# Optimization experiments

Measured on AMD Instinct MI355X. Metric: run time of the kernel, lower is better.

Reference implementation:

```python
import jax, jax.numpy as jnp
import numpy as np

N = 16384      # batch size
F = 1024       # n_features
H = 256        # n_dim (latent)


def setup_inputs() -> dict:
    key = jax.random.key(0)
    ks = jax.random.split(key, 6)
    X = jax.random.normal(ks[0], (N, F), dtype=jnp.float32)
    We = jax.random.normal(ks[1], (F, H), dtype=jnp.float32) / np.sqrt(F).astype(np.float32)
    be = jnp.zeros((H,), dtype=jnp.float32)
    Wd = jax.random.normal(ks[2], (H, F), dtype=jnp.float32) / np.sqrt(H).astype(np.float32)
    bd = jnp.zeros((F,), dtype=jnp.float32)
    Wc = jax.random.normal(ks[3], (H, 1), dtype=jnp.float32) / np.sqrt(H).astype(np.float32)
    bc = jnp.zeros((1,), dtype=jnp.float32)
    s = jax.random.randint(ks[4], (N,), 0, 2, dtype=jnp.int32)  # protected attribute labels in {0,1}
    return {"X": X, "We": We, "be": be, "Wd": Wd, "bd": bd, "Wc": Wc, "bc": bc, "s": s, "p": 1}


def reference(X, We, be, Wd, bd, Wc, bc, s, p):
    # encoder / decoder (single Linear each, as in the default NRL construction)
    g = X @ We + be                      # [N, H]
    rec = g @ Wd + bd                    # [N, F]
    mse_mean = jnp.mean((rec - X) ** 2)  # MSELoss is built with reduction='sum' but forward uses torch.mean(pow(...)) directly

    # critic scores for ALL rows (critics share weights: [module]*n_protected)
    c = (g @ Wc + bc)[:, 0]              # [N]

    # masked pairwise L1: sum_{i in P, j notin P} |c_i - c_j|
    mp = (s == p)                        # rows where s == p
    mpf = mp.astype(c.dtype)
    mrf = (~mp).astype(c.dtype)
    Dmat = jnp.abs(c[:, None] - c[None, :])   # [N, N] pairwise L1 (cdist equivalent)
    total = mpf @ (Dmat @ mrf)                # mp^T D mr == cdist(c_p, c_rest, p=1).sum()

    w_dist_count = mp.sum()                   # == w_dist.shape[0] (number of protected rows)
    w_dist_mean = total / w_dist_count.astype(c.dtype)

    return (mse_mean, jnp.asarray(rec.shape[0]), w_dist_mean, w_dist_count)
```

## Files before the change

kernel.cpp:

```cpp
#include <hip/hip_runtime.h>
#include <hip/hip_bf16.h>
#include <cstdint>

#define NR 16384
#define NF 1024
#define NH 256

typedef __bf16 bf16x8 __attribute__((ext_vector_type(8)));
typedef float f32x4 __attribute__((ext_vector_type(4)));
typedef unsigned short us8 __attribute__((ext_vector_type(8)));

static __device__ __forceinline__ unsigned short f2bf(float f) {
    unsigned u = __float_as_uint(f);
    u += 0x7FFFu + ((u >> 16) & 1u);
    return (unsigned short)(u >> 16);
}


__global__ __launch_bounds__(256) void prep_kernel(
    const float* __restrict__ We, const float* __restrict__ Wd,
    unsigned short* __restrict__ Wepk, unsigned short* __restrict__ Wdpk,
    float* __restrict__ hdr) {
    const int b = blockIdx.x, t = threadIdx.x;
    if (b == 0 && t < 192) hdr[t] = 0.f;
    const int lane = t & 63, q = lane >> 4, li = lane & 15, idx = t >> 6;
    if (b < 16) {
        const int nb = b;
#pragma unroll
        for (int p = 0; p < 8; p++) {
            const int kc = idx + 4 * p;
            us8 v;
#pragma unroll
            for (int e = 0; e < 8; e++)
                v[e] = f2bf(We[(size_t)(kc * 32 + q * 8 + e) * NH + nb * 16 + li]);
            *(us8*)&Wepk[((size_t)(nb * 32 + kc)) * 512 + lane * 8] = v;
        }
    } else {
        const int nb4 = b - 16;
#pragma unroll
        for (int p = 0; p < 8; p++) {
            const int c = nb4 * 32 + idx + 4 * p;
            const int nb = c >> 3, kc = c & 7;
            us8 v;
#pragma unroll
            for (int e = 0; e < 8; e++)
                v[e] = f2bf(Wd[(size_t)(kc * 32 + q * 8 + e) * NF + nb * 16 + li]);
            *(us8*)&Wdpk[((size_t)(nb * 8 + kc)) * 512 + lane * 8] = v;
        }
    }
}

__global__ __launch_bounds__(256) void fused_kernel(
    const float* __restrict__ X,
    const unsigned short* __restrict__ Wepk, const unsigned short* __restrict__ Wdpk,
    const float* __restrict__ be, const float* __restrict__ bd,
    const float* __restrict__ Wc, const int* __restrict__ s, const int* __restrict__ pv,
    float* __restrict__ cP, float* __restrict__ cR, float* __restrict__ hdr) {
    __shared__ union {
        unsigned short xa[16 * 1024];
        struct {
            unsigned short gs[16 * 256];
            float credu[4][16];
            float msred[4];
        } p2;
    } u;
    const int t = threadIdx.x;
    const int b = blockIdx.x, m0 = b * 16;
    const int w = t >> 6, lane = t & 63, q = lane >> 4, li = lane & 15;
    const int wn = w * 64;

    {
        const int r = t >> 4, cg = t & 15;
        const float* xrow = X + (size_t)(m0 + r) * NF + cg * 64;
#pragma unroll
        for (int ci = 0; ci < 8; ++ci) {
            float4 lo = *(const float4*)(xrow + ci * 8);
            float4 hi = *(const float4*)(xrow + ci * 8 + 4);
            us8 v;
            v[0] = f2bf(lo.x); v[1] = f2bf(lo.y); v[2] = f2bf(lo.z); v[3] = f2bf(lo.w);
            v[4] = f2bf(hi.x); v[5] = f2bf(hi.y); v[6] = f2bf(hi.z); v[7] = f2bf(hi.w);
            const int chl = cg * 8 + ci;
            *(us8*)&u.xa[r * 1024 + ((chl ^ r) & 127) * 8] = v;
        }
    }
    __syncthreads();

    const unsigned short* Bp[4];
#pragma unroll
    for (int j = 0; j < 4; j++)
        Bp[j] = Wepk + ((size_t)(w * 4 + j) * 32) * 512 + lane * 8;

    us8 fb[2][4];
#pragma unroll
    for (int z = 0; z < 2; ++z)
#pragma unroll
        for (int j = 0; j < 4; j++) fb[z][j] = *(const us8*)(Bp[j] + z * 512);

    f32x4 acc[4] = {};
#pragma unroll
    for (int kc = 0; kc < 32; ++kc) {
        const int cb = kc & 1;
        const int chl = kc * 4 + q;
        const int ph0 = (chl ^ li) & 127;
        bf16x8 a0 = __builtin_bit_cast(bf16x8, *(const us8*)&u.xa[li * 1024 + ph0 * 8]);
#pragma unroll
        for (int j = 0; j < 4; j++) {
            bf16x8 bf = __builtin_bit_cast(bf16x8, fb[cb][j]);
            acc[j] = __builtin_amdgcn_mfma_f32_16x16x32_bf16(bf, a0, acc[j], 0, 0, 0);
        }
        if (kc + 2 < 32) {
#pragma unroll
            for (int j = 0; j < 4; j++) fb[cb][j] = *(const us8*)(Bp[j] + (kc + 2) * 512);
        }
    }
    __syncthreads();

    const unsigned short* Wp = Wdpk + lane * 8;
    us8 gb[2][4];
#pragma unroll
    for (int z = 0; z < 2; ++z)
#pragma unroll
        for (int j = 0; j < 4; j++)
            gb[z][j] = *(const us8*)(Wp + ((size_t)((w * 4 + j) * 8 + z)) * 512);

    {
        float csum = 0.f;
        const int ml = li;
#pragma unroll
        for (int j = 0; j < 4; j++) {
            const int colb = wn + j * 16 + q * 4;
            float4 be4 = *(const float4*)&be[colb];
            float4 wc4 = *(const float4*)&Wc[colb];
            float v0 = acc[j][0] + be4.x;
            float v1 = acc[j][1] + be4.y;
            float v2 = acc[j][2] + be4.z;
            float v3 = acc[j][3] + be4.w;
            csum += v0 * wc4.x + v1 * wc4.y + v2 * wc4.z + v3 * wc4.w;
            ushort4 st = { f2bf(v0), f2bf(v1), f2bf(v2), f2bf(v3) };
            const int phys = (colb >> 3) ^ ml;
            *(ushort4*)&u.p2.gs[ml * 256 + phys * 8 + (q & 1) * 4] = st;
        }
        csum += __shfl_down(csum, 32);
        csum += __shfl_down(csum, 16);
        if (lane < 16) u.p2.credu[w][lane] = csum;
    }
    __syncthreads();

    if (t < 16) {
        float cs = u.p2.credu[0][t] + u.p2.credu[1][t] +
                   u.p2.credu[2][t] + u.p2.credu[3][t];
        bool pr = (s[m0 + t] == pv[0]);
        unsigned long long mk = __ballot(pr);
        int np = __popcll(mk);
        int baseP = 0, baseR = 0;
        if (t == 0) {
            baseP = atomicAdd((int*)hdr + 129, np);
            baseR = atomicAdd((int*)hdr + 130, 16 - np);
        }
        baseP = __shfl(baseP, 0);
        baseR = __shfl(baseR, 0);
        int offP = __popcll(mk & ((1ull << t) - 1ull));
        int offR = t - offP;
        if (pr) cP[baseP + offP] = cs; else cR[baseR + offR] = cs;
    }

    float lsum = 0.f;
    f32x4 a2[4] = {};
#pragma unroll
    for (int it = 0; it < 32; ++it) {
        const int cb = it & 1, pass = it >> 3, kc = it & 7;
        const int ml = li;
        const int phys = (kc * 4 + q) ^ ml;
        bf16x8 af = __builtin_bit_cast(bf16x8, *(const us8*)&u.p2.gs[ml * 256 + phys * 8]);
#pragma unroll
        for (int j = 0; j < 4; j++) {
            bf16x8 bf = __builtin_bit_cast(bf16x8, gb[cb][j]);
            a2[j] = __builtin_amdgcn_mfma_f32_16x16x32_bf16(bf, af, a2[j], 0, 0, 0);
        }
        if (it + 2 < 32) {
            const int p2i = (it + 2) >> 3, k2 = (it + 2) & 7;
#pragma unroll
            for (int j = 0; j < 4; j++)
                gb[cb][j] = *(const us8*)(Wp + ((size_t)((p2i * 16 + w * 4 + j) * 8 + k2)) * 512);
        }
        if (kc == 7) {
            const size_t rowoff = (size_t)(m0 + li) * NF;
#pragma unroll
            for (int j = 0; j < 4; j++) {
                const int colb = pass * 256 + wn + j * 16 + q * 4;
                float4 bd4 = *(const float4*)&bd[colb];
                float4 xr  = *(const float4*)&X[rowoff + colb];
                float d0 = a2[j][0] + bd4.x - xr.x;
                float d1 = a2[j][1] + bd4.y - xr.y;
                float d2 = a2[j][2] + bd4.z - xr.z;
                float d3 = a2[j][3] + bd4.w - xr.w;
                lsum += d0 * d0 + d1 * d1 + d2 * d2 + d3 * d3;
                a2[j] = (f32x4){0.f, 0.f, 0.f, 0.f};
            }
        }
    }
#pragma unroll
    for (int o = 32; o; o >>= 1) lsum += __shfl_down(lsum, o);
    if (lane == 0) u.p2.msred[w] = lsum;
    __syncthreads();
    if (t == 0)
        atomicAdd(&hdr[b & 63], u.p2.msred[0] + u.p2.msred[1] +
                                u.p2.msred[2] + u.p2.msred[3]);
}

__global__ __launch_bounds__(256) void pair_fin_kernel(
    const float* __restrict__ cP, const float* __restrict__ cR,
    float* __restrict__ hdr, float* __restrict__ out) {
    __shared__ float sj[1024];
    __shared__ float red[256];
    __shared__ int win;
    const int nP = ((const int*)hdr)[129];
    const int nR = ((const int*)hdr)[130];
    const int jb = blockIdx.x * 1024;
    int jn = nR - jb; if (jn < 0) jn = 0; if (jn > 1024) jn = 1024;
    float sum = 0.f;
    if (jn > 0 && blockIdx.y * 512 < nP) {
        for (int j = threadIdx.x; j < 1024; j += 256)
            sj[j] = (jb + j < nR) ? cR[jb + j] : 0.f;
        __syncthreads();
        const int a0 = blockIdx.y * 512 + threadIdx.x, a1 = a0 + 256;
        const float ca0 = (a0 < nP) ? cP[a0] : 0.f;
        const float ca1 = (a1 < nP) ? cP[a1] : 0.f;
        float s0 = 0.f, s1 = 0.f;
#pragma unroll 8
        for (int j4 = 0; j4 < 256; j4++) {
            float4 v = *(const float4*)&sj[j4 * 4];
            s0 += fabsf(ca0 - v.x) + fabsf(ca0 - v.y) + fabsf(ca0 - v.z) + fabsf(ca0 - v.w);
            s1 += fabsf(ca1 - v.x) + fabsf(ca1 - v.y) + fabsf(ca1 - v.z) + fabsf(ca1 - v.w);
        }
        float pad = (float)(1024 - jn);
        s0 -= pad * fabsf(ca0);
        s1 -= pad * fabsf(ca1);
        if (a0 >= nP) s0 = 0.f;
        if (a1 >= nP) s1 = 0.f;
        sum = s0 + s1;
#pragma unroll
        for (int o = 32; o; o >>= 1) sum += __shfl_down(sum, o);
        if ((threadIdx.x & 63) == 0 && sum != 0.f)
            atomicAdd(&hdr[64 + ((blockIdx.y * 16 + blockIdx.x) & 63)], sum);
    }
    __threadfence();
    __syncthreads();
    if (threadIdx.x == 0)
        win = (atomicAdd((int*)(hdr + 128), 1) == 16 * 32 - 1) ? 1 : 0;
    __syncthreads();
    if (win) {
        float v = (threadIdx.x < 128) ? atomicAdd(&hdr[threadIdx.x], 0.f) : 0.f;
        red[threadIdx.x] = v;
        __syncthreads();
        if (threadIdx.x == 0) {
            float ms = 0.f, ps = 0.f;
            for (int i = 0; i < 64; i++) { ms += red[i]; ps += red[64 + i]; }
            int np = atomicAdd((int*)(hdr + 129), 0);
            out[0] = ms / (float)((size_t)NR * NF);
            out[1] = (float)NR;
            out[2] = ps / (float)np;
            out[3] = (float)np;
        }
    }
}

extern "C" void kernel_launch(void* const* d_in, const int* in_sizes, int n_in,
                              void* d_out, int out_size, void* d_ws, size_t ws_size,
                              hipStream_t stream) {
    const float* X  = (const float*)d_in[0];
    const float* We = (const float*)d_in[1];
    const float* be = (const float*)d_in[2];
    const float* Wd = (const float*)d_in[3];
    const float* bd = (const float*)d_in[4];
    const float* Wc = (const float*)d_in[5];
    const int*   s  = (const int*)d_in[7];
    const int*   pv = (const int*)d_in[8];

    char* ws = (char*)d_ws;
    float* hdr = (float*)ws;
    float* cP  = (float*)(ws + 1024);
    float* cR  = (float*)(ws + 1024 + 65536);
    unsigned short* Wepk = (unsigned short*)(ws + 1024 + 2 * 65536);
    unsigned short* Wdpk = Wepk + (size_t)NH * NF;

    prep_kernel<<<32, 256, 0, stream>>>(We, Wd, Wepk, Wdpk, hdr);
    fused_kernel<<<1024, 256, 0, stream>>>(X, Wepk, Wdpk, be, bd, Wc, s, pv, cP, cR, hdr);
    pair_fin_kernel<<<dim3(16, 32), 256, 0, stream>>>(cP, cR, hdr, (float*)d_out);
}
```

Before: 214.4 us.

## Coalesce weight packing and X loads, deepen weight prefetch to four stages

The weight-packing kernel now runs 256 blocks, each thread handling one column, so global reads of We and Wd are coalesced across threads instead of strided. The X tile load is reorganized so each wave reads whole contiguous rows. In the fused kernel, the register prefetch ring for the packed weights grows from two to four stages to hide more global load latency. The deeper prefetch raises register pressure, which may reduce occupancy.

Measured after the change: 208.8 us. 2.6% less time.

```diff
diff --git a/kernel.cpp b/kernel.cpp
--- a/kernel.cpp
+++ b/kernel.cpp
@@ -23,30 +23,23 @@
     float* __restrict__ hdr) {
     const int b = blockIdx.x, t = threadIdx.x;
     if (b == 0 && t < 192) hdr[t] = 0.f;
-    const int lane = t & 63, q = lane >> 4, li = lane & 15, idx = t >> 6;
-    if (b < 16) {
-        const int nb = b;
-#pragma unroll
-        for (int p = 0; p < 8; p++) {
-            const int kc = idx + 4 * p;
-            us8 v;
-#pragma unroll
-            for (int e = 0; e < 8; e++)
-                v[e] = f2bf(We[(size_t)(kc * 32 + q * 8 + e) * NH + nb * 16 + li]);
-            *(us8*)&Wepk[((size_t)(nb * 32 + kc)) * 512 + lane * 8] = v;
-        }
+    if (b < 128) {
+        const int k0 = b, c = t;
+        const int kc = k0 >> 2, q = k0 & 3, nb = c >> 4, li = c & 15;
+        us8 v;
+#pragma unroll
+        for (int e = 0; e < 8; e++)
+            v[e] = f2bf(We[(size_t)(k0 * 8 + e) * NH + c]);
+        *(us8*)&Wepk[((size_t)(nb * 32 + kc)) * 512 + (q * 16 + li) * 8] = v;
     } else {
-        const int nb4 = b - 16;
-#pragma unroll
-        for (int p = 0; p < 8; p++) {
-            const int c = nb4 * 32 + idx + 4 * p;
-            const int nb = c >> 3, kc = c & 7;
-            us8 v;
-#pragma unroll
-            for (int e = 0; e < 8; e++)
-                v[e] = f2bf(Wd[(size_t)(kc * 32 + q * 8 + e) * NF + nb * 16 + li]);
-            *(us8*)&Wdpk[((size_t)(nb * 8 + kc)) * 512 + lane * 8] = v;
-        }
+        const int idx = b - 128;
+        const int k0 = idx >> 2, c = (idx & 3) * 256 + t;
+        const int kc = k0 >> 2, q = k0 & 3, nb = c >> 4, li = c & 15;
+        us8 v;
+#pragma unroll
+        for (int e = 0; e < 8; e++)
+            v[e] = f2bf(Wd[(size_t)(k0 * 8 + e) * NF + c]);
+        *(us8*)&Wdpk[((size_t)(nb * 8 + kc)) * 512 + (q * 16 + li) * 8] = v;
     }
 }
 
@@ -70,17 +63,20 @@
     const int wn = w * 64;
 
     {
-        const int r = t >> 4, cg = t & 15;
-        const float* xrow = X + (size_t)(m0 + r) * NF + cg * 64;
-#pragma unroll
-        for (int ci = 0; ci < 8; ++ci) {
-            float4 lo = *(const float4*)(xrow + ci * 8);
-            float4 hi = *(const float4*)(xrow + ci * 8 + 4);
-            us8 v;
-            v[0] = f2bf(lo.x); v[1] = f2bf(lo.y); v[2] = f2bf(lo.z); v[3] = f2bf(lo.w);
-            v[4] = f2bf(hi.x); v[5] = f2bf(hi.y); v[6] = f2bf(hi.z); v[7] = f2bf(hi.w);
-            const int chl = cg * 8 + ci;
-            *(us8*)&u.xa[r * 1024 + ((chl ^ r) & 127) * 8] = v;
+#pragma unroll
+        for (int rr = 0; rr < 4; ++rr) {
+            const int r = w * 4 + rr;
+            const float* xrow = X + (size_t)(m0 + r) * NF;
+#pragma unroll
+            for (int p = 0; p < 2; ++p) {
+                float4 lo = *(const float4*)(xrow + p * 512 + lane * 8);
+                float4 hi = *(const float4*)(xrow + p * 512 + lane * 8 + 4);
+                us8 v;
+                v[0] = f2bf(lo.x); v[1] = f2bf(lo.y); v[2] = f2bf(lo.z); v[3] = f2bf(lo.w);
+                v[4] = f2bf(hi.x); v[5] = f2bf(hi.y); v[6] = f2bf(hi.z); v[7] = f2bf(hi.w);
+                const int ch = p * 64 + lane;
+                *(us8*)&u.xa[r * 1024 + ((ch ^ r) & 127) * 8] = v;
+            }
         }
     }
     __syncthreads();
@@ -90,16 +86,16 @@
     for (int j = 0; j < 4; j++)
         Bp[j] = Wepk + ((size_t)(w * 4 + j) * 32) * 512 + lane * 8;
 
-    us8 fb[2][4];
-#pragma unroll
-    for (int z = 0; z < 2; ++z)
+    us8 fb[4][4];
+#pragma unroll
+    for (int z = 0; z < 4; ++z)
 #pragma unroll
         for (int j = 0; j < 4; j++) fb[z][j] = *(const us8*)(Bp[j] + z * 512);
 
     f32x4 acc[4] = {};
 #pragma unroll
     for (int kc = 0; kc < 32; ++kc) {
-        const int cb = kc & 1;
+        const int cb = kc & 3;
         const int chl = kc * 4 + q;
         const int ph0 = (chl ^ li) & 127;
         bf16x8 a0 = __builtin_bit_cast(bf16x8, *(const us8*)&u.xa[li * 1024 + ph0 * 8]);
@@ -108,17 +104,17 @@
             bf16x8 bf = __builtin_bit_cast(bf16x8, fb[cb][j]);
             acc[j] = __builtin_amdgcn_mfma_f32_16x16x32_bf16(bf, a0, acc[j], 0, 0, 0);
         }
-        if (kc + 2 < 32) {
-#pragma unroll
-            for (int j = 0; j < 4; j++) fb[cb][j] = *(const us8*)(Bp[j] + (kc + 2) * 512);
+        if (kc + 4 < 32) {
+#pragma unroll
+            for (int j = 0; j < 4; j++) fb[cb][j] = *(const us8*)(Bp[j] + (kc + 4) * 512);
         }
     }
     __syncthreads();
 
     const unsigned short* Wp = Wdpk + lane * 8;
-    us8 gb[2][4];
-#pragma unroll
-    for (int z = 0; z < 2; ++z)
+    us8 gb[4][4];
+#pragma unroll
+    for (int z = 0; z < 4; ++z)
 #pragma unroll
         for (int j = 0; j < 4; j++)
             gb[z][j] = *(const us8*)(Wp + ((size_t)((w * 4 + j) * 8 + z)) * 512);
@@ -168,7 +164,7 @@
     f32x4 a2[4] = {};
 #pragma unroll
     for (int it = 0; it < 32; ++it) {
-        const int cb = it & 1, pass = it >> 3, kc = it & 7;
+        const int cb = it & 3, pass = it >> 3, kc = it & 7;
         const int ml = li;
         const int phys = (kc * 4 + q) ^ ml;
         bf16x8 af = __builtin_bit_cast(bf16x8, *(const us8*)&u.p2.gs[ml * 256 + phys * 8]);
@@ -177,8 +173,8 @@
             bf16x8 bf = __builtin_bit_cast(bf16x8, gb[cb][j]);
             a2[j] = __builtin_amdgcn_mfma_f32_16x16x32_bf16(bf, af, a2[j], 0, 0, 0);
         }
-        if (it + 2 < 32) {
-            const int p2i = (it + 2) >> 3, k2 = (it + 2) & 7;
+        if (it + 4 < 32) {
+            const int p2i = (it + 4) >> 3, k2 = (it + 4) & 7;
 #pragma unroll
             for (int j = 0; j < 4; j++)
                 gb[cb][j] = *(const us8*)(Wp + ((size_t)((p2i * 16 + w * 4 + j) * 8 + k2)) * 512);
@@ -284,7 +280,7 @@
     unsigned short* Wepk = (unsigned short*)(ws + 1024 + 2 * 65536);
     unsigned short* Wdpk = Wepk + (size_t)NH * NF;
 
-    prep_kernel<<<32, 256, 0, stream>>>(We, Wd, Wepk, Wdpk, hdr);
+    prep_kernel<<<256, 256, 0, stream>>>(We, Wd, Wepk, Wdpk, hdr);
     fused_kernel<<<1024, 256, 0, stream>>>(X, Wepk, Wdpk, be, bd, Wc, s, pv, cP, cR, hdr);
     pair_fin_kernel<<<dim3(16, 32), 256, 0, stream>>>(cP, cR, hdr, (float*)d_out);
 }
```
